# Kernel tuning notes

Measured on AMD Instinct MI355X. Metric: run time of the kernel, lower is better.

## Reference

```python
import jax, jax.numpy as jnp
import numpy as np

N = 50000
E = 800000
NEG_SLOPE = 0.2
BN_EPS = 1e-5


def _bn(x, g, b, m, v):
    # BatchNorm1d in eval mode (running stats)
    return (x - m) * (g * jax.lax.rsqrt(v + BN_EPS)) + b


def _gat_conv(x, src, dst, W, a_src, a_dst, bias, heads, hid):
    n = x.shape[0]
    h = (x @ W).reshape(n, heads, hid)                      # [N,H,D]
    s_src = jnp.sum(h * a_src, axis=-1)                     # [N,H]
    s_dst = jnp.sum(h * a_dst, axis=-1)                     # [N,H]
    score = jax.nn.leaky_relu(s_src[src] + s_dst[dst], NEG_SLOPE)  # [E,H]
    # segment softmax over incoming edges of each dst node, per head
    mx = jax.ops.segment_max(score, dst, num_segments=n)
    ex = jnp.exp(score - mx[dst])
    sm = jax.ops.segment_sum(ex, dst, num_segments=n)
    alpha = ex / sm[dst]                                    # [E,H]
    msg = h[src] * alpha[:, :, None]                        # [E,H,D]
    out = jax.ops.segment_sum(msg, dst, num_segments=n)     # [N,H,D]
    return out.reshape(n, heads * hid) + bias


def setup_inputs() -> dict:
    key = jax.random.key(0)
    ks = jax.random.split(key, 16)
    d_in, heads, hid = 64, 8, 32
    wdim = heads * hid  # 256
    inp = {
        "x": jax.random.normal(ks[0], (N, d_in), jnp.float32),
        "edge_index": jax.random.randint(ks[1], (2, E), 0, N, jnp.int32),
        "bn1_g": jnp.ones((d_in,), jnp.float32),
        "bn1_b": jnp.zeros((d_in,), jnp.float32),
        "bn1_m": jnp.zeros((d_in,), jnp.float32),
        "bn1_v": jnp.ones((d_in,), jnp.float32),
        "W1": jax.random.normal(ks[2], (d_in, wdim), jnp.float32) * (1.0 / np.sqrt(d_in)),
        "a1_src": jax.random.normal(ks[3], (heads, hid), jnp.float32) * 0.1,
        "a1_dst": jax.random.normal(ks[4], (heads, hid), jnp.float32) * 0.1,
        "b1": jnp.zeros((wdim,), jnp.float32),
        "bn2_g": jnp.ones((wdim,), jnp.float32),
        "bn2_b": jnp.zeros((wdim,), jnp.float32),
        "bn2_m": jnp.zeros((wdim,), jnp.float32),
        "bn2_v": jnp.ones((wdim,), jnp.float32),
        "W2": jax.random.normal(ks[5], (wdim, wdim), jnp.float32) * (1.0 / np.sqrt(wdim)),
        "a2_src": jax.random.normal(ks[6], (heads, hid), jnp.float32) * 0.1,
        "a2_dst": jax.random.normal(ks[7], (heads, hid), jnp.float32) * 0.1,
        "b2": jnp.zeros((wdim,), jnp.float32),
        "bn3_g": jnp.ones((wdim,), jnp.float32),
        "bn3_b": jnp.zeros((wdim,), jnp.float32),
        "bn3_m": jnp.zeros((wdim,), jnp.float32),
        "bn3_v": jnp.ones((wdim,), jnp.float32),
        "skip_W": jax.random.normal(ks[8], (d_in, wdim), jnp.float32) * (1.0 / np.sqrt(d_in)),
        "skip_b": jnp.zeros((wdim,), jnp.float32),
        "p1_W": jax.random.normal(ks[9], (wdim, hid), jnp.float32) * (1.0 / np.sqrt(wdim)),
        "p1_b": jnp.zeros((hid,), jnp.float32),
        "p2_W": jax.random.normal(ks[10], (hid, 1), jnp.float32) * (1.0 / np.sqrt(hid)),
        "p2_b": jnp.zeros((1,), jnp.float32),
    }
    return inp


def reference(x, edge_index, bn1_g, bn1_b, bn1_m, bn1_v, W1, a1_src, a1_dst, b1,
              bn2_g, bn2_b, bn2_m, bn2_v, W2, a2_src, a2_dst, b2,
              bn3_g, bn3_b, bn3_m, bn3_v, skip_W, skip_b, p1_W, p1_b, p2_W, p2_b):
    heads, hid = 8, 32
    n = x.shape[0]
    # add self loops once (PyG GATConv default add_self_loops=True)
    loops = jnp.arange(n, dtype=edge_index.dtype)
    src = jnp.concatenate([edge_index[0], loops])
    dst = jnp.concatenate([edge_index[1], loops])

    x_in = x
    h = _bn(x, bn1_g, bn1_b, bn1_m, bn1_v)
    h = jax.nn.elu(_gat_conv(h, src, dst, W1, a1_src, a1_dst, b1, heads, hid))
    h = _bn(h, bn2_g, bn2_b, bn2_m, bn2_v)
    h = jax.nn.elu(_gat_conv(h, src, dst, W2, a2_src, a2_dst, b2, heads, hid))
    h = _bn(h, bn3_g, bn3_b, bn3_m, bn3_v)
    h = h + (x_in @ skip_W + skip_b)
    h = jax.nn.relu(h @ p1_W + p1_b)
    return h @ p2_W + p2_b  # [N, 1]
```

## Files before the change

kernel.cpp:

```cpp
#include <hip/hip_runtime.h>
#include <hip/hip_bf16.h>
#include <math.h>
#include <stdint.h>

#define HID 256
#define HEADS 8
#define BN_EPS 1e-5f
#define NEG 0.2f
#define WCAP 96
#define SEPT 8
#define SCHUNK (256 * SEPT)

typedef _Float16 hv8 __attribute__((ext_vector_type(8)));
typedef __fp16 fv2 __attribute__((ext_vector_type(2)));
typedef float f32x4 __attribute__((ext_vector_type(4)));

__device__ __forceinline__ float lrelu(float x) { return x > 0.f ? x : NEG * x; }
__device__ __forceinline__ float eluf(float x)  { return x > 0.f ? x : __expf(x) - 1.f; }

__device__ __forceinline__ unsigned short f2h(float f) {
    _Float16 h = (_Float16)f;
    union { _Float16 h; unsigned short u; } c; c.h = h;
    return c.u;
}
__device__ __forceinline__ unsigned int pk2h(float lo, float hi) {
    return (unsigned int)f2h(lo) | ((unsigned int)f2h(hi) << 16);
}
__device__ __forceinline__ unsigned int pkrtz(float lo, float hi) {
    fv2 r = __builtin_amdgcn_cvt_pkrtz(lo, hi);
    union { fv2 h; unsigned int u; } c; c.h = r;
    return c.u;
}

#define FMAMIX_LO(acc, pk, al) \
    asm("v_fma_mix_f32 %0, %1, %2, %0 op_sel:[0,0,0] op_sel_hi:[1,0,0]" \
        : "+v"(acc) : "v"(pk), "v"(al))
#define FMAMIX_HI(acc, pk, al) \
    asm("v_fma_mix_f32 %0, %1, %2, %0 op_sel:[1,0,0] op_sel_hi:[1,0,0]" \
        : "+v"(acc) : "v"(pk), "v"(al))
#define FMAMIX4(q, al) \
    FMAMIX_LO(a0, q.x, al); FMAMIX_HI(a1, q.x, al); \
    FMAMIX_LO(a2, q.y, al); FMAMIX_HI(a3, q.y, al); \
    FMAMIX_LO(a4, q.z, al); FMAMIX_HI(a5, q.z, al); \
    FMAMIX_LO(a6, q.w, al); FMAMIX_HI(a7, q.w, al)


__global__ __launch_bounds__(256) void scan1_kernel(const int* __restrict__ deg,
                                                    int* __restrict__ bsum, int N) {
    __shared__ int part[256];
    int t = threadIdx.x;
    int base = blockIdx.x * SCHUNK + t * SEPT;
    int s = 0;
    if (base + SEPT <= N) {
        int4 a = *(const int4*)&deg[base];
        int4 c = *(const int4*)&deg[base + 4];
        s = a.x + a.y + a.z + a.w + c.x + c.y + c.z + c.w;
    } else {
#pragma unroll
        for (int i = 0; i < SEPT; ++i) {
            int j = base + i;
            if (j < N) s += deg[j];
        }
    }
    part[t] = s;
    __syncthreads();
    for (int d = 128; d > 0; d >>= 1) {
        if (t < d) part[t] += part[t + d];
        __syncthreads();
    }
    if (t == 0) bsum[blockIdx.x] = part[0];
}

__global__ __launch_bounds__(256) void scan2_kernel(int* __restrict__ bsum,
                                                    int* __restrict__ offs,
                                                    int nb, int N) {
    __shared__ int part[256];
    int t = threadIdx.x;
    int v = (t < nb) ? bsum[t] : 0;
    part[t] = v;
    __syncthreads();
    for (int d = 1; d < 256; d <<= 1) {
        int o = (t >= d) ? part[t - d] : 0;
        __syncthreads();
        part[t] += o;
        __syncthreads();
    }
    if (t < nb) bsum[t] = part[t] - v;
    if (t == 255) offs[N] = part[255];
}

__global__ __launch_bounds__(256) void scan3_kernel(const int* __restrict__ deg,
                                                    const int* __restrict__ bsum,
                                                    int* __restrict__ offs, int N) {
    __shared__ int part[256];
    int t = threadIdx.x;
    int base = blockIdx.x * SCHUNK + t * SEPT;
    int loc[SEPT];
    int s = 0;
#pragma unroll
    for (int i = 0; i < SEPT; ++i) {
        int j = base + i;
        int d = (j < N) ? deg[j] : 0;
        loc[i] = s;
        s += d;
    }
    part[t] = s;
    __syncthreads();
    for (int d = 1; d < 256; d <<= 1) {
        int o = (t >= d) ? part[t - d] : 0;
        __syncthreads();
        part[t] += o;
        __syncthreads();
    }
    int ex = part[t] - s + bsum[blockIdx.x];
#pragma unroll
    for (int i = 0; i < SEPT; ++i) {
        int j = base + i;
        if (j < N) offs[j] = ex + loc[i];
    }
}

__global__ __launch_bounds__(256) void scatter_kernel(const int* __restrict__ ei,
                                                      const int* __restrict__ offs,
                                                      int* __restrict__ cur,
                                                      int* __restrict__ csr_src,
                                                      int E, int EE) {
    int e = blockIdx.x * 256 + threadIdx.x;
    if (e >= EE) return;
    int s = (e < E) ? ei[e] : (e - E);
    int d = (e < E) ? ei[E + e] : (e - E);
    int pos = offs[d] + atomicAdd(&cur[d], 1);
    csr_src[pos] = s;
}

__global__ __launch_bounds__(32) void sfold_kernel(const float* __restrict__ skip_W,
                                                   const float* __restrict__ p1_W,
                                                   float* __restrict__ Sp) {
    int cx = blockIdx.x, j = threadIdx.x;
    float acc = 0.f;
    for (int c = 0; c < HID; c += 4) {
        float4 sw = *(const float4*)&skip_W[(size_t)cx * HID + c];
        acc = fmaf(sw.x, p1_W[(c + 0) * 32 + j], acc);
        acc = fmaf(sw.y, p1_W[(c + 1) * 32 + j], acc);
        acc = fmaf(sw.z, p1_W[(c + 2) * 32 + j], acc);
        acc = fmaf(sw.w, p1_W[(c + 3) * 32 + j], acc);
    }
    Sp[cx * 32 + j] = acc;
}

__device__ __forceinline__ void wfrag_body(const float* __restrict__ W,
                                           const float* __restrict__ g,
                                           const float* __restrict__ v,
                                           unsigned short* __restrict__ frag,
                                           int tile, int l) {
    int ct = tile & 15, kt = tile >> 4;
    int c = ct * 16 + (l & 15);
    int k0 = kt * 32 + (l >> 4) * 8;
    float val[8];
#pragma unroll
    for (int j = 0; j < 8; ++j) {
        float s = g[k0 + j] * rsqrtf(v[k0 + j] + BN_EPS);
        val[j] = W[(size_t)(k0 + j) * HID + c] * s;
    }
    uint4 o;
    o.x = pk2h(val[0], val[1]);
    o.y = pk2h(val[2], val[3]);
    o.z = pk2h(val[4], val[5]);
    o.w = pk2h(val[6], val[7]);
    *(uint4*)&frag[((size_t)tile * 64 + l) * 8] = o;
}

__global__ __launch_bounds__(256) void prep_kernel(
    const float* __restrict__ W1, const float* __restrict__ bn1_g,
    const float* __restrict__ bn1_b, const float* __restrict__ bn1_m,
    const float* __restrict__ bn1_v,
    const float* __restrict__ W2, const float* __restrict__ bn2_g,
    const float* __restrict__ bn2_b, const float* __restrict__ bn2_m,
    const float* __restrict__ bn2_v,
    const float* __restrict__ g3, const float* __restrict__ b3,
    const float* __restrict__ m3, const float* __restrict__ v3,
    const float* __restrict__ Sp, const float* __restrict__ skip_b,
    const float* __restrict__ p1_W, const float* __restrict__ p1_b,
    unsigned short* __restrict__ wf1, unsigned short* __restrict__ wf2,
    unsigned short* __restrict__ hf, float* __restrict__ c1,
    float* __restrict__ c2, float* __restrict__ cp,
    const int* __restrict__ ei, int* __restrict__ deg, int E, int EE) {
    int b = blockIdx.x;
    int tid = threadIdx.x;

    if (b >= 48) {
        int e = (b - 48) * 256 + tid;
        if (e < EE) {
            int d = (e < E) ? ei[E + e] : (e - E);
            atomicAdd(&deg[d], 1);
        }
        return;
    }

    int sub = tid >> 6, l = tid & 63;
    if (b < 8) {
        wfrag_body(W1, bn1_g, bn1_v, wf1, b * 4 + sub, l);
    } else if (b < 40) {
        wfrag_body(W2, bn2_g, bn2_v, wf2, (b - 8) * 4 + sub, l);
    } else if (b < 45) {
        int tile = (b - 40) * 4 + sub;
        int mt = tile & 1, kt = tile >> 1;
        int j = mt * 16 + (l & 15);
        int k0 = kt * 32 + (l >> 4) * 8;
        float val[8];
#pragma unroll
        for (int jj = 0; jj < 8; ++jj) {
            int c = k0 + jj;
            if (c < HID) {
                float s3 = g3[c] * rsqrtf(v3[c] + BN_EPS);
                val[jj] = s3 * p1_W[c * 32 + j];
            } else {
                val[jj] = Sp[(c - HID) * 32 + j];
            }
        }
        uint4 o;
        o.x = pk2h(val[0], val[1]);
        o.y = pk2h(val[2], val[3]);
        o.z = pk2h(val[4], val[5]);
        o.w = pk2h(val[6], val[7]);
        *(uint4*)&hf[((size_t)tile * 64 + l) * 8] = o;
    } else if (b == 45) {
        float acc = 0.f;
        for (int k = 0; k < 64; ++k) {
            float s = bn1_g[k] * rsqrtf(bn1_v[k] + BN_EPS);
            acc = fmaf(bn1_b[k] - bn1_m[k] * s, W1[(size_t)k * HID + tid], acc);
        }
        c1[tid] = acc;
    } else if (b == 46) {
        float acc = 0.f;
        for (int k = 0; k < HID; ++k) {
            float s = bn2_g[k] * rsqrtf(bn2_v[k] + BN_EPS);
            acc = fmaf(bn2_b[k] - bn2_m[k] * s, W2[(size_t)k * HID + tid], acc);
        }
        c2[tid] = acc;
    } else {
        if (tid < 32) {
            float acc = p1_b[tid];
            for (int c = 0; c < HID; ++c) {
                float s3 = g3[c] * rsqrtf(v3[c] + BN_EPS);
                acc = fmaf(b3[c] - m3[c] * s3 + skip_b[c], p1_W[c * 32 + tid], acc);
            }
            cp[tid] = acc;
        }
    }
}

template <int K, bool F16IN>
__global__ __launch_bounds__(256) void gemm_mfma(
    const float* __restrict__ inf, const unsigned short* __restrict__ inh,
    const unsigned short* __restrict__ wfrag, const float* __restrict__ cvec,
    const float* __restrict__ a_src, const float* __restrict__ a_dst,
    unsigned short* __restrict__ h, float* __restrict__ s_src,
    float* __restrict__ s_dst, int N) {
    constexpr int KT = K / 32;
    constexpr int OPR = K / 8;
    __shared__ unsigned short xfrag[KT * 4 * 64 * 8];
    int tid = threadIdx.x;
    int w = tid >> 6, l = tid & 63;
    int gg = l >> 4, li = l & 15;
    int base = blockIdx.x * 64;

    for (int id = tid; id < 64 * OPR; id += 256) {
        int r = id / OPR, o = id % OPR;
        int node = min(base + r, N - 1);
        uint4 pkv;
        if constexpr (F16IN) {
            pkv = *(const uint4*)&inh[(size_t)node * K + o * 8];
        } else {
            const float* p = &inf[(size_t)node * K + o * 8];
            float4 f0 = *(const float4*)p;
            float4 f1 = *(const float4*)(p + 4);
            pkv.x = pkrtz(f0.x, f0.y);
            pkv.y = pkrtz(f0.z, f0.w);
            pkv.z = pkrtz(f1.x, f1.y);
            pkv.w = pkrtz(f1.z, f1.w);
        }
        int kt = o >> 2, og = o & 3, nt = r >> 4;
        *(uint4*)&xfrag[(((kt * 4 + nt) * 64) + (r & 15) + 16 * og) * 8] = pkv;
    }
    __syncthreads();

    f32x4 acc[4][4];
#pragma unroll
    for (int mm = 0; mm < 4; ++mm) {
        float4 cv = *(const float4*)&cvec[64 * w + 16 * mm + 4 * gg];
#pragma unroll
        for (int nn = 0; nn < 4; ++nn) {
            acc[mm][nn][0] = cv.x; acc[mm][nn][1] = cv.y;
            acc[mm][nn][2] = cv.z; acc[mm][nn][3] = cv.w;
        }
    }

    for (int ks = 0; ks < KT; ++ks) {
        hv8 a[4], b[4];
#pragma unroll
        for (int mm = 0; mm < 4; ++mm)
            a[mm] = *(const hv8*)&wfrag[((size_t)(ks * 16 + w * 4 + mm) * 64 + l) * 8];
#pragma unroll
        for (int nn = 0; nn < 4; ++nn)
            b[nn] = *(const hv8*)&xfrag[((ks * 4 + nn) * 64 + l) * 8];
#pragma unroll
        for (int mm = 0; mm < 4; ++mm)
#pragma unroll
            for (int nn = 0; nn < 4; ++nn)
                acc[mm][nn] = __builtin_amdgcn_mfma_f32_16x16x32_f16(
                    a[mm], b[nn], acc[mm][nn], 0, 0, 0);
    }

    float svp[4][2], sdp[4][2];
#pragma unroll
    for (int nn = 0; nn < 4; ++nn) { svp[nn][0]=0.f; svp[nn][1]=0.f; sdp[nn][0]=0.f; sdp[nn][1]=0.f; }

#pragma unroll
    for (int mm = 0; mm < 4; ++mm) {
        int cb = 64 * w + 16 * mm + 4 * gg;
        float4 as4 = *(const float4*)&a_src[cb];
        float4 ad4 = *(const float4*)&a_dst[cb];
        int hp = mm >> 1;
#pragma unroll
        for (int nn = 0; nn < 4; ++nn) {
            f32x4 A = acc[mm][nn];
            svp[nn][hp] += A[0]*as4.x + A[1]*as4.y + A[2]*as4.z + A[3]*as4.w;
            sdp[nn][hp] += A[0]*ad4.x + A[1]*ad4.y + A[2]*ad4.z + A[3]*ad4.w;
            int node = base + 16 * nn + li;
            if (node < N) {
                uint2 pkv2;
                pkv2.x = pkrtz(A[0], A[1]);
                pkv2.y = pkrtz(A[2], A[3]);
                *(uint2*)&h[(size_t)node * HID + cb] = pkv2;
            }
        }
    }
#pragma unroll
    for (int nn = 0; nn < 4; ++nn)
#pragma unroll
        for (int hp = 0; hp < 2; ++hp) {
            svp[nn][hp] += __shfl_xor(svp[nn][hp], 16);
            svp[nn][hp] += __shfl_xor(svp[nn][hp], 32);
            sdp[nn][hp] += __shfl_xor(sdp[nn][hp], 16);
            sdp[nn][hp] += __shfl_xor(sdp[nn][hp], 32);
        }
    if (gg == 0) {
#pragma unroll
        for (int nn = 0; nn < 4; ++nn) {
            int node = base + 16 * nn + li;
            if (node < N) {
#pragma unroll
                for (int hp = 0; hp < 2; ++hp) {
                    s_src[node * HEADS + 2 * w + hp] = svp[nn][hp];
                    s_dst[node * HEADS + 2 * w + hp] = sdp[nn][hp];
                }
            }
        }
    }
}

__global__ __launch_bounds__(256) void agg_kernel(
    const unsigned short* __restrict__ h, const float* __restrict__ s_src,
    const float* __restrict__ s_dst, const int* __restrict__ offs,
    const int* __restrict__ csr_src, const float* __restrict__ bias,
    unsigned short* __restrict__ outp, int N) {
    __shared__ float al_lds[4][WCAP][8];
    __shared__ int   u_lds[4][WCAP];
    __shared__ float mi_lds[4][16];
    int tid = threadIdx.x;
    int w = tid >> 6, l = tid & 63;
    int vtx = blockIdx.x * 4 + w;
    if (vtx >= N) return;
    int beg = offs[vtx], end = offs[vtx + 1];
    int deg = end - beg;
    int dc = min(deg, WCAP);

    int headA = l & 7, slot = l >> 3;
    float sdv = s_dst[vtx * HEADS + headA];

    float m = -3.0e38f;
    for (int e = slot; e < deg; e += 8) {
        int u = csr_src[beg + e];
        float sc = lrelu(s_src[u * HEADS + headA] + sdv);
        if (e < WCAP) {
            if (headA == 0) u_lds[w][e] = u;
            al_lds[w][e][headA] = sc;
        }
        m = fmaxf(m, sc);
    }
    m = fmaxf(m, __shfl_xor(m, 8));
    m = fmaxf(m, __shfl_xor(m, 16));
    m = fmaxf(m, __shfl_xor(m, 32));

    float s = 0.f;
    for (int e = slot; e < dc; e += 8) {
        float p = __expf(al_lds[w][e][headA] - m);
        al_lds[w][e][headA] = p;
        s += p;
    }
    for (int e = WCAP + slot; e < deg; e += 8) {
        int u = csr_src[beg + e];
        s += __expf(lrelu(s_src[u * HEADS + headA] + sdv) - m);
    }
    s += __shfl_xor(s, 8);
    s += __shfl_xor(s, 16);
    s += __shfl_xor(s, 32);
    if (slot == 0) {
        mi_lds[w][headA] = m;
        mi_lds[w][8 + headA] = 1.f / s;
    }
    __builtin_amdgcn_wave_barrier();

    int grp = l >> 5, gl = l & 31;
    int hd = gl >> 2;
    float a0 = 0.f, a1 = 0.f, a2 = 0.f, a3 = 0.f;
    float a4 = 0.f, a5 = 0.f, a6 = 0.f, a7 = 0.f;
    const unsigned short* hb = h + 8 * gl;
    int e = grp;
    for (; e + 6 < dc; e += 8) {
        int u0 = u_lds[w][e];
        int u1 = u_lds[w][e + 2];
        int u2 = u_lds[w][e + 4];
        int u3 = u_lds[w][e + 6];
        float l0 = al_lds[w][e][hd];
        float l1 = al_lds[w][e + 2][hd];
        float l2 = al_lds[w][e + 4][hd];
        float l3 = al_lds[w][e + 6][hd];
        uint4 v0 = *(const uint4*)&hb[(size_t)u0 * HID];
        uint4 v1 = *(const uint4*)&hb[(size_t)u1 * HID];
        uint4 v2 = *(const uint4*)&hb[(size_t)u2 * HID];
        uint4 v3 = *(const uint4*)&hb[(size_t)u3 * HID];
        FMAMIX4(v0, l0);
        FMAMIX4(v1, l1);
        FMAMIX4(v2, l2);
        FMAMIX4(v3, l3);
    }
    for (; e < dc; e += 2) {
        int u0 = u_lds[w][e];
        float l0 = al_lds[w][e][hd];
        uint4 v0 = *(const uint4*)&hb[(size_t)u0 * HID];
        FMAMIX4(v0, l0);
    }
    if (deg > WCAP) {
        float mh = mi_lds[w][hd];
        float sdh = s_dst[vtx * HEADS + hd];
        for (int ee = WCAP + grp; ee < deg; ee += 2) {
            int u = csr_src[beg + ee];
            float al = __expf(lrelu(s_src[u * HEADS + hd] + sdh) - mh);
            uint4 v0 = *(const uint4*)&hb[(size_t)u * HID];
            FMAMIX4(v0, al);
        }
    }
    a0 += __shfl_xor(a0, 32); a1 += __shfl_xor(a1, 32);
    a2 += __shfl_xor(a2, 32); a3 += __shfl_xor(a3, 32);
    a4 += __shfl_xor(a4, 32); a5 += __shfl_xor(a5, 32);
    a6 += __shfl_xor(a6, 32); a7 += __shfl_xor(a7, 32);

    float inv = mi_lds[w][8 + hd];
    float e0 = grp ? a4 : a0;
    float e1 = grp ? a5 : a1;
    float e2 = grp ? a6 : a2;
    float e3 = grp ? a7 : a3;
    float4 bb = *(const float4*)&bias[8 * gl + 4 * grp];
    uint2 ov;
    ov.x = pkrtz(eluf(e0 * inv + bb.x), eluf(e1 * inv + bb.y));
    ov.y = pkrtz(eluf(e2 * inv + bb.z), eluf(e3 * inv + bb.w));
    *(uint2*)&outp[(size_t)vtx * HID + 8 * gl + 4 * grp] = ov;
}

__global__ __launch_bounds__(256) void final_mfma(
    const unsigned short* __restrict__ t_in, const float* __restrict__ x,
    const unsigned short* __restrict__ hf, const float* __restrict__ cp,
    const float* __restrict__ p2_W, const float* __restrict__ p2_b,
    float* __restrict__ outp, int N) {
    constexpr int KT = 10;
    __shared__ unsigned short xfrag[KT * 4 * 64 * 8];
    int tid = threadIdx.x;
    int w = tid >> 6, l = tid & 63;
    int gg = l >> 4, li = l & 15;
    int base = blockIdx.x * 64;

    for (int id = tid; id < 64 * 40; id += 256) {
        int r = id / 40, o = id % 40;
        int node = min(base + r, N - 1);
        uint4 pkv;
        if (o < 32) {
            pkv = *(const uint4*)&t_in[(size_t)node * HID + o * 8];
        } else {
            const float* p = &x[(size_t)node * 64 + (o - 32) * 8];
            float4 f0 = *(const float4*)p;
            float4 f1 = *(const float4*)(p + 4);
            pkv.x = pkrtz(f0.x, f0.y);
            pkv.y = pkrtz(f0.z, f0.w);
            pkv.z = pkrtz(f1.x, f1.y);
            pkv.w = pkrtz(f1.z, f1.w);
        }
        int kt = o >> 2, og = o & 3, nt = r >> 4;
        *(uint4*)&xfrag[(((kt * 4 + nt) * 64) + (r & 15) + 16 * og) * 8] = pkv;
    }
    __syncthreads();

    f32x4 acc[2];
#pragma unroll
    for (int mt = 0; mt < 2; ++mt) {
        float4 cv = *(const float4*)&cp[mt * 16 + 4 * gg];
        acc[mt][0] = cv.x; acc[mt][1] = cv.y; acc[mt][2] = cv.z; acc[mt][3] = cv.w;
    }

    for (int kt = 0; kt < KT; ++kt) {
        hv8 b = *(const hv8*)&xfrag[((kt * 4 + w) * 64 + l) * 8];
#pragma unroll
        for (int mt = 0; mt < 2; ++mt) {
            hv8 a = *(const hv8*)&hf[((size_t)(kt * 2 + mt) * 64 + l) * 8];
            acc[mt] = __builtin_amdgcn_mfma_f32_16x16x32_f16(a, b, acc[mt], 0, 0, 0);
        }
    }

    float po = 0.f;
#pragma unroll
    for (int mt = 0; mt < 2; ++mt) {
        float4 p2v = *(const float4*)&p2_W[mt * 16 + 4 * gg];
        po += fmaxf(acc[mt][0], 0.f) * p2v.x;
        po += fmaxf(acc[mt][1], 0.f) * p2v.y;
        po += fmaxf(acc[mt][2], 0.f) * p2v.z;
        po += fmaxf(acc[mt][3], 0.f) * p2v.w;
    }
    po += __shfl_xor(po, 16);
    po += __shfl_xor(po, 32);
    int node = base + 16 * w + li;
    if (gg == 0 && node < N) outp[node] = po + p2_b[0];
}


extern "C" void kernel_launch(void* const* d_in, const int* in_sizes, int n_in,
                              void* d_out, int out_size, void* d_ws, size_t ws_size,
                              hipStream_t stream) {
    const float* x      = (const float*)d_in[0];
    const int*   ei     = (const int*)  d_in[1];
    const float* bn1_g  = (const float*)d_in[2];
    const float* bn1_b  = (const float*)d_in[3];
    const float* bn1_m  = (const float*)d_in[4];
    const float* bn1_v  = (const float*)d_in[5];
    const float* W1     = (const float*)d_in[6];
    const float* a1_src = (const float*)d_in[7];
    const float* a1_dst = (const float*)d_in[8];
    const float* b1     = (const float*)d_in[9];
    const float* bn2_g  = (const float*)d_in[10];
    const float* bn2_b  = (const float*)d_in[11];
    const float* bn2_m  = (const float*)d_in[12];
    const float* bn2_v  = (const float*)d_in[13];
    const float* W2     = (const float*)d_in[14];
    const float* a2_src = (const float*)d_in[15];
    const float* a2_dst = (const float*)d_in[16];
    const float* b2     = (const float*)d_in[17];
    const float* bn3_g  = (const float*)d_in[18];
    const float* bn3_b  = (const float*)d_in[19];
    const float* bn3_m  = (const float*)d_in[20];
    const float* bn3_v  = (const float*)d_in[21];
    const float* skip_W = (const float*)d_in[22];
    const float* skip_b = (const float*)d_in[23];
    const float* p1_W   = (const float*)d_in[24];
    const float* p1_b   = (const float*)d_in[25];
    const float* p2_W   = (const float*)d_in[26];
    const float* p2_b   = (const float*)d_in[27];

    int N = in_sizes[0] / 64;
    int E = in_sizes[1] / 2;
    int EE = E + N;

    uintptr_t w = (uintptr_t)d_ws;
    auto carve = [&](size_t bytes) -> void* {
        uintptr_t p = w;
        w += (bytes + 255) & ~(size_t)255;
        return (void*)p;
    };
    int*   deg  = (int*)carve((size_t)N * 4);
    int*   cur  = (int*)carve((size_t)N * 4);
    int*   offs = (int*)carve(((size_t)N + 1) * 4);
    int*   csr  = (int*)carve((size_t)EE * 4);
    int*   bsum = (int*)carve((size_t)256 * 4);
    float* ssrc = (float*)carve((size_t)N * HEADS * 4);
    float* sdst = (float*)carve((size_t)N * HEADS * 4);
    unsigned short* wf1 = (unsigned short*)carve((size_t)2 * 16 * 64 * 8 * 2);
    unsigned short* wf2 = (unsigned short*)carve((size_t)8 * 16 * 64 * 8 * 2);
    unsigned short* hf  = (unsigned short*)carve((size_t)20 * 64 * 8 * 2);
    float* c1   = (float*)carve((size_t)HID * 4);
    float* c2   = (float*)carve((size_t)HID * 4);
    float* cp   = (float*)carve((size_t)32 * 4);
    float* Sp   = (float*)carve((size_t)64 * 32 * 4);
    unsigned short* hbf = (unsigned short*)carve((size_t)N * HID * 2);
    unsigned short* tbuf = (unsigned short*)carve((size_t)N * HID * 2);

    hipMemsetAsync(deg, 0, ((size_t)N * 4 + 255 & ~(size_t)255) + (size_t)N * 4, stream);

    sfold_kernel<<<64, 32, 0, stream>>>(skip_W, p1_W, Sp);
    int eblk = (EE + 255) / 256;
    prep_kernel<<<48 + eblk, 256, 0, stream>>>(
        W1, bn1_g, bn1_b, bn1_m, bn1_v,
        W2, bn2_g, bn2_b, bn2_m, bn2_v,
        bn3_g, bn3_b, bn3_m, bn3_v, Sp, skip_b, p1_W, p1_b,
        wf1, wf2, hf, c1, c2, cp, ei, deg, E, EE);

    int nb = (N + SCHUNK - 1) / SCHUNK;
    scan1_kernel<<<nb, 256, 0, stream>>>(deg, bsum, N);
    scan2_kernel<<<1, 256, 0, stream>>>(bsum, offs, nb, N);
    scan3_kernel<<<nb, 256, 0, stream>>>(deg, bsum, offs, N);
    scatter_kernel<<<eblk, 256, 0, stream>>>(ei, offs, cur, csr, E, EE);

    int gblk = (N + 63) / 64;
    int ablk = (N + 3) / 4;
    gemm_mfma<64, false><<<gblk, 256, 0, stream>>>(x, nullptr, wf1, c1,
                                                   a1_src, a1_dst,
                                                   hbf, ssrc, sdst, N);
    agg_kernel<<<ablk, 256, 0, stream>>>(hbf, ssrc, sdst, offs, csr, b1, tbuf, N);

    gemm_mfma<HID, true><<<gblk, 256, 0, stream>>>(nullptr, tbuf, wf2, c2,
                                                   a2_src, a2_dst,
                                                   hbf, ssrc, sdst, N);
    agg_kernel<<<ablk, 256, 0, stream>>>(hbf, ssrc, sdst, offs, csr, b2, tbuf, N);

    final_mfma<<<gblk, 256, 0, stream>>>(tbuf, x, hf, cp, p2_W, p2_b,
                                         (float*)d_out, N);
}
```

Measured before the change: 296.6 us.

## Reorder layer-1 GAT to aggregate raw features before per-head projection

```diff
diff --git a/kernel.cpp b/kernel.cpp
--- a/kernel.cpp
+++ b/kernel.cpp
@@ -171,9 +171,11 @@
 }
 
 __global__ __launch_bounds__(256) void prep_kernel(
+    const float* __restrict__ x,
     const float* __restrict__ W1, const float* __restrict__ bn1_g,
     const float* __restrict__ bn1_b, const float* __restrict__ bn1_m,
-    const float* __restrict__ bn1_v,
+    const float* __restrict__ bn1_v, const float* __restrict__ b1,
+    const float* __restrict__ a1s, const float* __restrict__ a1d,
     const float* __restrict__ W2, const float* __restrict__ bn2_g,
     const float* __restrict__ bn2_b, const float* __restrict__ bn2_m,
     const float* __restrict__ bn2_v,
@@ -182,17 +184,33 @@
     const float* __restrict__ Sp, const float* __restrict__ skip_b,
     const float* __restrict__ p1_W, const float* __restrict__ p1_b,
     unsigned short* __restrict__ wf1, unsigned short* __restrict__ wf2,
-    unsigned short* __restrict__ hf, float* __restrict__ c1,
-    float* __restrict__ c2, float* __restrict__ cp,
-    const int* __restrict__ ei, int* __restrict__ deg, int E, int EE) {
+    unsigned short* __restrict__ hf, float* __restrict__ c1raw,
+    float* __restrict__ c1t, float* __restrict__ c2, float* __restrict__ cp,
+    float* __restrict__ ws, unsigned short* __restrict__ xh,
+    const int* __restrict__ ei, int* __restrict__ deg, int E, int EE, int N) {
     int b = blockIdx.x;
     int tid = threadIdx.x;
 
-    if (b >= 48) {
-        int e = (b - 48) * 256 + tid;
-        if (e < EE) {
-            int d = (e < E) ? ei[E + e] : (e - E);
-            atomicAdd(&deg[d], 1);
+    if (b >= 49) {
+        int eb = (EE + 255) / 256;
+        if (b < 49 + eb) {
+            int e = (b - 49) * 256 + tid;
+            if (e < EE) {
+                int d = (e < E) ? ei[E + e] : (e - E);
+                atomicAdd(&deg[d], 1);
+            }
+        } else {
+            size_t idx = ((size_t)(b - 49 - eb) * 256 + tid) * 8;
+            if (idx < (size_t)N * 64) {
+                float4 f0 = *(const float4*)&x[idx];
+                float4 f1 = *(const float4*)&x[idx + 4];
+                uint4 o;
+                o.x = pkrtz(f0.x, f0.y);
+                o.y = pkrtz(f0.z, f0.w);
+                o.z = pkrtz(f1.x, f1.y);
+                o.w = pkrtz(f1.z, f1.w);
+                *(uint4*)&xh[idx] = o;
+            }
         }
         return;
     }
@@ -230,7 +248,8 @@
             float s = bn1_g[k] * rsqrtf(bn1_v[k] + BN_EPS);
             acc = fmaf(bn1_b[k] - bn1_m[k] * s, W1[(size_t)k * HID + tid], acc);
         }
-        c1[tid] = acc;
+        c1raw[tid] = acc;
+        c1t[tid] = acc + b1[tid];
     } else if (b == 46) {
         float acc = 0.f;
         for (int k = 0; k < HID; ++k) {
@@ -238,7 +257,7 @@
             acc = fmaf(bn2_b[k] - bn2_m[k] * s, W2[(size_t)k * HID + tid], acc);
         }
         c2[tid] = acc;
-    } else {
+    } else if (b == 47) {
         if (tid < 32) {
             float acc = p1_b[tid];
             for (int c = 0; c < HID; ++c) {
@@ -247,12 +266,59 @@
             }
             cp[tid] = acc;
         }
-    }
-}
-
-template <int K, bool F16IN>
+    } else {
+#pragma unroll
+        for (int q = 0; q < 4; ++q) {
+            int idx = q * 256 + tid;
+            int k = idx >> 4, out = idx & 15;
+            int head = out & 7;
+            const float* av = (out < 8) ? a1s : a1d;
+            float s1k = bn1_g[k] * rsqrtf(bn1_v[k] + BN_EPS);
+            float acc = 0.f;
+            for (int d = 0; d < 32; ++d)
+                acc = fmaf(s1k * W1[(size_t)k * HID + head * 32 + d],
+                           av[head * 32 + d], acc);
+            ws[k * 16 + out] = acc;
+        }
+    }
+}
+
+__global__ __launch_bounds__(256) void s1_kernel(
+    const float* __restrict__ x, const float* __restrict__ ws,
+    const float* __restrict__ c1raw, const float* __restrict__ a1s,
+    const float* __restrict__ a1d, float* __restrict__ ssrc,
+    float* __restrict__ sdst, int N) {
+    __shared__ float xs[64][64];
+    int tid = threadIdx.x;
+    int base = blockIdx.x * 64;
+    for (int id = tid; id < 64 * 16; id += 256) {
+        int r = id >> 4, q = id & 15;
+        int node = min(base + r, N - 1);
+        *(float4*)&xs[r][q * 4] = *(const float4*)&x[(size_t)node * 64 + q * 4];
+    }
+    __syncthreads();
+#pragma unroll
+    for (int q = 0; q < 4; ++q) {
+        int idx = q * 256 + tid;
+        int r = idx >> 4, out = idx & 15;
+        int head = out & 7;
+        const float* av = (out < 8) ? a1s : a1d;
+        float acc = 0.f;
+        for (int k = 0; k < 64; ++k)
+            acc = fmaf(xs[r][k], ws[k * 16 + out], acc);
+        for (int d = 0; d < 32; ++d)
+            acc = fmaf(c1raw[head * 32 + d], av[head * 32 + d], acc);
+        int node = base + r;
+        if (node < N) {
+            if (out < 8) ssrc[node * HEADS + head] = acc;
+            else         sdst[node * HEADS + head] = acc;
+        }
+    }
+}
+
+template <int K>
 __global__ __launch_bounds__(256) void gemm_mfma(
-    const float* __restrict__ inf, const unsigned short* __restrict__ inh,
+    const unsigned short* __restrict__ inh,
     const unsigned short* __restrict__ wfrag, const float* __restrict__ cvec,
     const float* __restrict__ a_src, const float* __restrict__ a_dst,
     unsigned short* __restrict__ h, float* __restrict__ s_src,
@@ -268,18 +334,7 @@
     for (int id = tid; id < 64 * OPR; id += 256) {
         int r = id / OPR, o = id % OPR;
         int node = min(base + r, N - 1);
-        uint4 pkv;
-        if constexpr (F16IN) {
-            pkv = *(const uint4*)&inh[(size_t)node * K + o * 8];
-        } else {
-            const float* p = &inf[(size_t)node * K + o * 8];
-            float4 f0 = *(const float4*)p;
-            float4 f1 = *(const float4*)(p + 4);
-            pkv.x = pkrtz(f0.x, f0.y);
-            pkv.y = pkrtz(f0.z, f0.w);
-            pkv.z = pkrtz(f1.x, f1.y);
-            pkv.w = pkrtz(f1.z, f1.w);
-        }
+        uint4 pkv = *(const uint4*)&inh[(size_t)node * K + o * 8];
         int kt = o >> 2, og = o & 3, nt = r >> 4;
         *(uint4*)&xfrag[(((kt * 4 + nt) * 64) + (r & 15) + 16 * og) * 8] = pkv;
     }
@@ -360,6 +415,69 @@
     }
 }
 
+__global__ __launch_bounds__(256) void xgemm_kernel(
+    const unsigned short* __restrict__ xagg, const unsigned short* __restrict__ wf1,
+    const float* __restrict__ c1t, unsigned short* __restrict__ t, int N) {
+    __shared__ unsigned short xfrag[16 * 2 * 64 * 8];
+    int tid = threadIdx.x;
+    int w = tid >> 6, l = tid & 63;
+    int gg = l >> 4, li = l & 15;
+    int base = blockIdx.x * 32;
+
+    for (int id = tid; id < 32 * 64; id += 256) {
+        int r = id >> 6, o = id & 63;
+        int node = min(base + r, N - 1);
+        uint4 pkv = *(const uint4*)&xagg[(size_t)node * 512 + o * 8];
+        int kt = o >> 2, og = o & 3, nt = r >> 4;
+        *(uint4*)&xfrag[(((kt * 2 + nt) * 64) + (r & 15) + 16 * og) * 8] = pkv;
+    }
+    __syncthreads();
+
+    f32x4 acc[4][2];
+#pragma unroll
+    for (int mm = 0; mm < 4; ++mm) {
+        float4 cv = *(const float4*)&c1t[64 * w + 16 * mm + 4 * gg];
+#pragma unroll
+        for (int nn = 0; nn < 2; ++nn) {
+            acc[mm][nn][0] = cv.x; acc[mm][nn][1] = cv.y;
+            acc[mm][nn][2] = cv.z; acc[mm][nn][3] = cv.w;
+        }
+    }
+
+#pragma unroll
+    for (int mm = 0; mm < 4; ++mm) {
+        int ct = w * 4 + mm;
+        int head = ct >> 1;
+#pragma unroll
+        for (int kt1 = 0; kt1 < 2; ++kt1) {
+            hv8 a = *(const hv8*)&wf1[((size_t)(kt1 * 16 + ct) * 64 + l) * 8];
+            int ktg = head * 2 + kt1;
+#pragma unroll
+            for (int nn = 0; nn < 2; ++nn) {
+                hv8 b = *(const hv8*)&xfrag[((ktg * 2 + nn) * 64 + l) * 8];
+                acc[mm][nn] = __builtin_amdgcn_mfma_f32_16x16x32_f16(a, b, acc[mm][nn], 0, 0, 0);
+            }
+        }
+    }
+
+#pragma unroll
+    for (int mm = 0; mm < 4; ++mm) {
+        int cb = 64 * w + 16 * mm + 4 * gg;
+#pragma unroll
+        for (int nn = 0; nn < 2; ++nn) {
+            int node = base + 16 * nn + li;
+            if (node < N) {
+                f32x4 A = acc[mm][nn];
+                uint2 pkv2;
+                pkv2.x = pkrtz(eluf(A[0]), eluf(A[1]));
+                pkv2.y = pkrtz(eluf(A[2]), eluf(A[3]));
+                *(uint2*)&t[(size_t)node * HID + cb] = pkv2;
+            }
+        }
+    }
+}
+
+template <int XAGG>
 __global__ __launch_bounds__(256) void agg_kernel(
     const unsigned short* __restrict__ h, const float* __restrict__ s_src,
     const float* __restrict__ s_dst, const int* __restrict__ offs,
@@ -412,61 +530,109 @@
     }
     __builtin_amdgcn_wave_barrier();
 
-    int grp = l >> 5, gl = l & 31;
-    int hd = gl >> 2;
     float a0 = 0.f, a1 = 0.f, a2 = 0.f, a3 = 0.f;
     float a4 = 0.f, a5 = 0.f, a6 = 0.f, a7 = 0.f;
-    const unsigned short* hb = h + 8 * gl;
-    int e = grp;
-    for (; e + 6 < dc; e += 8) {
-        int u0 = u_lds[w][e];
-        int u1 = u_lds[w][e + 2];
-        int u2 = u_lds[w][e + 4];
-        int u3 = u_lds[w][e + 6];
-        float l0 = al_lds[w][e][hd];
-        float l1 = al_lds[w][e + 2][hd];
-        float l2 = al_lds[w][e + 4][hd];
-        float l3 = al_lds[w][e + 6][hd];
-        uint4 v0 = *(const uint4*)&hb[(size_t)u0 * HID];
-        uint4 v1 = *(const uint4*)&hb[(size_t)u1 * HID];
-        uint4 v2 = *(const uint4*)&hb[(size_t)u2 * HID];
-        uint4 v3 = *(const uint4*)&hb[(size_t)u3 * HID];
-        FMAMIX4(v0, l0);
-        FMAMIX4(v1, l1);
-        FMAMIX4(v2, l2);
-        FMAMIX4(v3, l3);
-    }
-    for (; e < dc; e += 2) {
-        int u0 = u_lds[w][e];
-        float l0 = al_lds[w][e][hd];
-        uint4 v0 = *(const uint4*)&hb[(size_t)u0 * HID];
-        FMAMIX4(v0, l0);
-    }
-    if (deg > WCAP) {
-        float mh = mi_lds[w][hd];
-        float sdh = s_dst[vtx * HEADS + hd];
-        for (int ee = WCAP + grp; ee < deg; ee += 2) {
-            int u = csr_src[beg + ee];
-            float al = __expf(lrelu(s_src[u * HEADS + hd] + sdh) - mh);
-            uint4 v0 = *(const uint4*)&hb[(size_t)u * HID];
-            FMAMIX4(v0, al);
-        }
-    }
-    a0 += __shfl_xor(a0, 32); a1 += __shfl_xor(a1, 32);
-    a2 += __shfl_xor(a2, 32); a3 += __shfl_xor(a3, 32);
-    a4 += __shfl_xor(a4, 32); a5 += __shfl_xor(a5, 32);
-    a6 += __shfl_xor(a6, 32); a7 += __shfl_xor(a7, 32);
-
-    float inv = mi_lds[w][8 + hd];
-    float e0 = grp ? a4 : a0;
-    float e1 = grp ? a5 : a1;
-    float e2 = grp ? a6 : a2;
-    float e3 = grp ? a7 : a3;
-    float4 bb = *(const float4*)&bias[8 * gl + 4 * grp];
-    uint2 ov;
-    ov.x = pkrtz(eluf(e0 * inv + bb.x), eluf(e1 * inv + bb.y));
-    ov.y = pkrtz(eluf(e2 * inv + bb.z), eluf(e3 * inv + bb.w));
-    *(uint2*)&outp[(size_t)vtx * HID + 8 * gl + 4 * grp] = ov;
+
+    if (XAGG) {
+        int hh = l >> 3, db = (l & 7) * 8;
+        const unsigned short* xb = h + db;
+        int e = 0;
+        for (; e + 3 < dc; e += 4) {
+            int u0 = u_lds[w][e];
+            int u1 = u_lds[w][e + 1];
+            int u2 = u_lds[w][e + 2];
+            int u3 = u_lds[w][e + 3];
+            float l0 = al_lds[w][e][hh];
+            float l1 = al_lds[w][e + 1][hh];
+            float l2 = al_lds[w][e + 2][hh];
+            float l3 = al_lds[w][e + 3][hh];
+            uint4 v0 = *(const uint4*)&xb[(size_t)u0 * 64];
+            uint4 v1 = *(const uint4*)&xb[(size_t)u1 * 64];
+            uint4 v2 = *(const uint4*)&xb[(size_t)u2 * 64];
+            uint4 v3 = *(const uint4*)&xb[(size_t)u3 * 64];
+            FMAMIX4(v0, l0);
+            FMAMIX4(v1, l1);
+            FMAMIX4(v2, l2);
+            FMAMIX4(v3, l3);
+        }
+        for (; e < dc; ++e) {
+            int u0 = u_lds[w][e];
+            float l0 = al_lds[w][e][hh];
+            uint4 v0 = *(const uint4*)&xb[(size_t)u0 * 64];
+            FMAMIX4(v0, l0);
+        }
+        if (deg > WCAP) {
+            float mh = mi_lds[w][hh];
+            float sdh = s_dst[vtx * HEADS + hh];
+            for (int ee = WCAP; ee < deg; ++ee) {
+                int u = csr_src[beg + ee];
+                float al = __expf(lrelu(s_src[u * HEADS + hh] + sdh) - mh);
+                uint4 v0 = *(const uint4*)&xb[(size_t)u * 64];
+                FMAMIX4(v0, al);
+            }
+        }
+        float inv = mi_lds[w][8 + hh];
+        uint4 ov;
+        ov.x = pkrtz(a0 * inv, a1 * inv);
+        ov.y = pkrtz(a2 * inv, a3 * inv);
+        ov.z = pkrtz(a4 * inv, a5 * inv);
+        ov.w = pkrtz(a6 * inv, a7 * inv);
+        *(uint4*)&outp[(size_t)vtx * 512 + hh * 64 + db] = ov;
+    } else {
+        int grp = l >> 5, gl = l & 31;
+        int hd = gl >> 2;
+        const unsigned short* hb = h + 8 * gl;
+        int e = grp;
+        for (; e + 6 < dc; e += 8) {
+            int u0 = u_lds[w][e];
+            int u1 = u_lds[w][e + 2];
+            int u2 = u_lds[w][e + 4];
+            int u3 = u_lds[w][e + 6];
+            float l0 = al_lds[w][e][hd];
+            float l1 = al_lds[w][e + 2][hd];
+            float l2 = al_lds[w][e + 4][hd];
+            float l3 = al_lds[w][e + 6][hd];
+            uint4 v0 = *(const uint4*)&hb[(size_t)u0 * HID];
+            uint4 v1 = *(const uint4*)&hb[(size_t)u1 * HID];
+            uint4 v2 = *(const uint4*)&hb[(size_t)u2 * HID];
+            uint4 v3 = *(const uint4*)&hb[(size_t)u3 * HID];
+            FMAMIX4(v0, l0);
+            FMAMIX4(v1, l1);
+            FMAMIX4(v2, l2);
+            FMAMIX4(v3, l3);
+        }
+        for (; e < dc; e += 2) {
+            int u0 = u_lds[w][e];
+            float l0 = al_lds[w][e][hd];
+            uint4 v0 = *(const uint4*)&hb[(size_t)u0 * HID];
+            FMAMIX4(v0, l0);
+        }
+        if (deg > WCAP) {
+            float mh = mi_lds[w][hd];
+            float sdh = s_dst[vtx * HEADS + hd];
+            for (int ee = WCAP + grp; ee < deg; ee += 2) {
+                int u = csr_src[beg + ee];
+                float al = __expf(lrelu(s_src[u * HEADS + hd] + sdh) - mh);
+                uint4 v0 = *(const uint4*)&hb[(size_t)u * HID];
+                FMAMIX4(v0, al);
+            }
+        }
+        a0 += __shfl_xor(a0, 32); a1 += __shfl_xor(a1, 32);
+        a2 += __shfl_xor(a2, 32); a3 += __shfl_xor(a3, 32);
+        a4 += __shfl_xor(a4, 32); a5 += __shfl_xor(a5, 32);
+        a6 += __shfl_xor(a6, 32); a7 += __shfl_xor(a7, 32);
+
+        float inv = mi_lds[w][8 + hd];
+        float e0 = grp ? a4 : a0;
+        float e1 = grp ? a5 : a1;
+        float e2 = grp ? a6 : a2;
+        float e3 = grp ? a7 : a3;
+        float4 bb = *(const float4*)&bias[8 * gl + 4 * grp];
+        uint2 ov;
+        ov.x = pkrtz(eluf(e0 * inv + bb.x), eluf(e1 * inv + bb.y));
+        ov.y = pkrtz(eluf(e2 * inv + bb.z), eluf(e3 * inv + bb.w));
+        *(uint2*)&outp[(size_t)vtx * HID + 8 * gl + 4 * grp] = ov;
+    }
 }
 
 __global__ __launch_bounds__(256) void final_mfma(
@@ -585,22 +751,27 @@
     unsigned short* wf1 = (unsigned short*)carve((size_t)2 * 16 * 64 * 8 * 2);
     unsigned short* wf2 = (unsigned short*)carve((size_t)8 * 16 * 64 * 8 * 2);
     unsigned short* hf  = (unsigned short*)carve((size_t)20 * 64 * 8 * 2);
-    float* c1   = (float*)carve((size_t)HID * 4);
-    float* c2   = (float*)carve((size_t)HID * 4);
-    float* cp   = (float*)carve((size_t)32 * 4);
-    float* Sp   = (float*)carve((size_t)64 * 32 * 4);
-    unsigned short* hbf = (unsigned short*)carve((size_t)N * HID * 2);
+    float* c1raw = (float*)carve((size_t)HID * 4);
+    float* c1t   = (float*)carve((size_t)HID * 4);
+    float* c2    = (float*)carve((size_t)HID * 4);
+    float* cp    = (float*)carve((size_t)32 * 4);
+    float* Sp    = (float*)carve((size_t)64 * 32 * 4);
+    float* ws    = (float*)carve((size_t)64 * 16 * 4);
+    unsigned short* xh   = (unsigned short*)carve((size_t)N * 64 * 2);
+    unsigned short* xagg = (unsigned short*)carve((size_t)N * 512 * 2);
+    unsigned short* hbf  = (unsigned short*)carve((size_t)N * HID * 2);
     unsigned short* tbuf = (unsigned short*)carve((size_t)N * HID * 2);
 
     hipMemsetAsync(deg, 0, ((size_t)N * 4 + 255 & ~(size_t)255) + (size_t)N * 4, stream);
 
     sfold_kernel<<<64, 32, 0, stream>>>(skip_W, p1_W, Sp);
     int eblk = (EE + 255) / 256;
-    prep_kernel<<<48 + eblk, 256, 0, stream>>>(
-        W1, bn1_g, bn1_b, bn1_m, bn1_v,
+    int cblk = (N * 64 / 8 + 255) / 256;
+    prep_kernel<<<49 + eblk + cblk, 256, 0, stream>>>(
+        x, W1, bn1_g, bn1_b, bn1_m, bn1_v, b1, a1_src, a1_dst,
         W2, bn2_g, bn2_b, bn2_m, bn2_v,
         bn3_g, bn3_b, bn3_m, bn3_v, Sp, skip_b, p1_W, p1_b,
-        wf1, wf2, hf, c1, c2, cp, ei, deg, E, EE);
+        wf1, wf2, hf, c1raw, c1t, c2, cp, ws, xh, ei, deg, E, EE, N);
 
     int nb = (N + SCHUNK - 1) / SCHUNK;
     scan1_kernel<<<nb, 256, 0, stream>>>(deg, bsum, N);
@@ -610,15 +781,18 @@
 
     int gblk = (N + 63) / 64;
     int ablk = (N + 3) / 4;
-    gemm_mfma<64, false><<<gblk, 256, 0, stream>>>(x, nullptr, wf1, c1,
-                                                   a1_src, a1_dst,
-                                                   hbf, ssrc, sdst, N);
-    agg_kernel<<<ablk, 256, 0, stream>>>(hbf, ssrc, sdst, offs, csr, b1, tbuf, N);
-
-    gemm_mfma<HID, true><<<gblk, 256, 0, stream>>>(nullptr, tbuf, wf2, c2,
-                                                   a2_src, a2_dst,
-                                                   hbf, ssrc, sdst, N);
-    agg_kernel<<<ablk, 256, 0, stream>>>(hbf, ssrc, sdst, offs, csr, b2, tbuf, N);
+    int xblk = (N + 31) / 32;
+
+    s1_kernel<<<gblk, 256, 0, stream>>>(x, ws, c1raw, a1_src, a1_dst,
+                                        ssrc, sdst, N);
+    agg_kernel<1><<<ablk, 256, 0, stream>>>(xh, ssrc, sdst, offs, csr,
+                                            nullptr, xagg, N);
+    xgemm_kernel<<<xblk, 256, 0, stream>>>(xagg, wf1, c1t, tbuf, N);
+
+    gemm_mfma<HID><<<gblk, 256, 0, stream>>>(tbuf, wf2, c2, a2_src, a2_dst,
+                                             hbf, ssrc, sdst, N);
+    agg_kernel<0><<<ablk, 256, 0, stream>>>(hbf, ssrc, sdst, offs, csr,
+                                            b2, tbuf, N);
 
     final_mfma<<<gblk, 256, 0, stream>>>(tbuf, x, hf, cp, p2_W, p2_b,
                                          (float*)d_out, N);
```

New measurement: 324.3 us. +9.3%, slower.
